# Kernel optimization log

Measured on AMD Instinct MI355X. Metric: run time of the kernel, lower is better.

## Reference

```python
import jax, jax.numpy as jnp
import numpy as np

K = 100
TEMPERATURE = 1.0


def setup_inputs() -> dict:
    key = jax.random.key(0)
    k1, k2, k3 = jax.random.split(key, 3)
    student_emb = jax.random.normal(k1, (8, 512, 1500), dtype=jnp.float32)
    teacher_codes = jax.random.randint(k2, (8, 1500), 0, 4096, dtype=jnp.int64)
    codebook = jax.random.normal(k3, (4096, 512), dtype=jnp.float32)
    return {"student_emb": student_emb, "teacher_codes": teacher_codes, "codebook": codebook}


def reference(student_emb, teacher_codes, codebook):
    B, C, T = student_emb.shape
    # flatten tokens: (N, C) with N = B*T
    emb = jnp.transpose(student_emb, (0, 2, 1)).reshape(-1, C)
    codes = teacher_codes.reshape(-1).astype(jnp.int32)

    # Euclidean cdist via the ||a||^2 + ||b||^2 - 2ab expansion (same math as torch.cdist)
    emb_sq = jnp.sum(emb * emb, axis=1, keepdims=True)            # (N,1)
    cb_sq = jnp.sum(codebook * codebook, axis=1)[None, :]         # (1,V)
    d2 = emb_sq + cb_sq - 2.0 * jnp.matmul(emb, codebook.T)       # (N,V)
    distances = jnp.sqrt(jnp.maximum(d2, 0.0))

    # top-k smallest distances
    _, top_k_indices = jax.lax.top_k(-distances, K)               # (N,K)

    # include_correct: replace last candidate with the true code if absent
    correct_in_topk = jnp.any(top_k_indices == codes[:, None], axis=1)
    top_k_indices = top_k_indices.at[:, -1].set(
        jnp.where(correct_in_topk, top_k_indices[:, -1], codes))

    candidate_distances = jnp.take_along_axis(distances, top_k_indices, axis=1)
    logits = -candidate_distances / TEMPERATURE                   # (N,K)

    match = top_k_indices == codes[:, None]
    local_labels = jnp.argmax(match.astype(jnp.int32), axis=1)    # (N,)

    logp = jax.nn.log_softmax(logits, axis=1)
    loss = -jnp.mean(jnp.take_along_axis(logp, local_labels[:, None], axis=1))

    local_predictions = jnp.argmax(logits, axis=-1)
    local_accuracy = jnp.mean((local_predictions == local_labels).astype(jnp.float32))
    global_predictions = jnp.argmin(distances, axis=-1)
    global_accuracy = jnp.mean((global_predictions == codes).astype(jnp.float32))
    correct_in_candidates = jnp.mean(jnp.any(top_k_indices == codes[:, None], axis=1).astype(jnp.float32))

    return loss, local_accuracy, global_accuracy, correct_in_candidates
```

## Files before the change

### kernel.cpp

```cpp
#include <hip/hip_runtime.h>
#include <hip/hip_bf16.h>
#include <cstdint>

#define B_ 8
#define C_ 512
#define T_ 1500
#define N_ (B_*T_)
#define NPAD_ 12032
#define V_ 4096
#define K_ 100

typedef unsigned long long u64;
typedef __attribute__((ext_vector_type(8))) short short8;
typedef __attribute__((ext_vector_type(8))) unsigned short u16x8;
typedef __attribute__((ext_vector_type(4))) float f32x4;

__device__ __forceinline__ unsigned short f2bf(float x){
    __hip_bfloat16 h = __float2bfloat16(x);
    return __builtin_bit_cast(unsigned short, h);
}
__device__ __forceinline__ unsigned short f2h(float x){
    return __builtin_bit_cast(unsigned short, (_Float16)x);
}
__device__ __forceinline__ float h2f(unsigned short h){
    return (float)__builtin_bit_cast(_Float16, h);
}

__device__ __forceinline__ void gll16(const unsigned short* g, unsigned short* l){
    __builtin_amdgcn_global_load_lds(
        (const __attribute__((address_space(1))) void*)g,
        (__attribute__((address_space(3))) void*)l, 16, 0, 0);
}

__global__ __launch_bounds__(256) void cbconv_kernel(const float* __restrict__ CB,
                                                     unsigned short* __restrict__ CBh,
                                                     float* __restrict__ csq){
    int wv = threadIdx.x >> 6, lane = threadIdx.x & 63;
    int r = blockIdx.x * 4 + wv;
    const float4* p4 = (const float4*)(CB + (size_t)r * C_);
    ushort4* o4 = (ushort4*)(CBh + (size_t)r * C_);
    float s = 0.f;
    #pragma unroll
    for (int j = 0; j < 2; ++j){
        float4 v = p4[lane + j*64];
        s += v.x*v.x + v.y*v.y + v.z*v.z + v.w*v.w;
        ushort4 h; h.x = f2bf(v.x); h.y = f2bf(v.y); h.z = f2bf(v.z); h.w = f2bf(v.w);
        o4[lane + j*64] = h;
    }
    #pragma unroll
    for (int o = 32; o; o >>= 1) s += __shfl_down(s, o, 64);
    if (lane == 0) csq[r] = s;
}

__global__ __launch_bounds__(256) void transpose_conv_kernel(const float* __restrict__ S,
                                                             unsigned short* __restrict__ embT,
                                                             float* __restrict__ esq){
    __shared__ float tile[32][33];
    __shared__ float psum[8][33];
    int b  = blockIdx.z;
    int c0 = blockIdx.y * 32;
    int t0 = blockIdx.x * 32;
    int tx = threadIdx.x, ty = threadIdx.y;
    #pragma unroll
    for (int r = 0; r < 4; ++r){
        int c = c0 + ty + r*8;
        int t = t0 + tx;
        tile[ty + r*8][tx] = (t < T_) ? S[((size_t)b*C_ + c)*T_ + t] : 0.f;
    }
    __syncthreads();
    float ps = 0.f;
    #pragma unroll
    for (int r = 0; r < 4; ++r){ float v = tile[ty + r*8][tx]; ps += v * v; }
    psum[ty][tx] = ps;
    #pragma unroll
    for (int r = 0; r < 4; ++r){
        int t = t0 + ty + r*8;
        int c = c0 + tx;
        if (t < T_) embT[((size_t)b*T_ + t)*C_ + c] = f2bf(tile[tx][ty + r*8]);
    }
    __syncthreads();
    if (ty == 0){
        int t = t0 + tx;
        if (t < T_){
            float s2 = 0.f;
            #pragma unroll
            for (int w = 0; w < 8; ++w) s2 += psum[w][tx];
            atomicAdd(&esq[b*T_ + t], s2);
        }
    }
}

__global__ __launch_bounds__(256) void gemm_dot_kernel(
    const unsigned short* __restrict__ A, const unsigned short* __restrict__ Bm,
    unsigned short* __restrict__ doth, int row_lo, int row_hi)
{
    __shared__ unsigned short smem[128*136];
    unsigned short* As = smem;
    unsigned short* Bs = smem + 128*32;
    int tid = threadIdx.x, lane = tid & 63, wv = tid >> 6;
    int row0 = row_lo + blockIdx.x * 128;
    int col0 = blockIdx.y * 128;

    int sr = lane >> 2;
    int sk = (lane & 3) * 8;
    int ar0 = row0 + wv*32 + sr;       int ar1 = ar0 + 16;
    int ca0 = (ar0 < N_) ? ar0 : N_-1; int ca1 = (ar1 < N_) ? ar1 : N_-1;
    const unsigned short* Ap0 = A  + (size_t)ca0 * C_ + sk;
    const unsigned short* Ap1 = A  + (size_t)ca1 * C_ + sk;
    const unsigned short* Bp0 = Bm + (size_t)(col0 + wv*32 + sr) * C_ + sk;
    const unsigned short* Bp1 = Bp0 + (size_t)16 * C_;
    unsigned short* Ad0 = &As[(wv*32     ) * 32];
    unsigned short* Ad1 = &As[(wv*32 + 16) * 32];
    unsigned short* Bd0 = &Bs[(wv*32     ) * 32];
    unsigned short* Bd1 = &Bs[(wv*32 + 16) * 32];

    int wm = (wv >> 1) * 64, wn = (wv & 1) * 64;
    int fr = lane & 15;
    int fk = (lane >> 4) * 8;

    f32x4 acc[4][4];
    #pragma unroll
    for (int i = 0; i < 4; ++i)
        #pragma unroll
        for (int j = 0; j < 4; ++j) acc[i][j] = (f32x4){0.f, 0.f, 0.f, 0.f};

    for (int kt = 0; kt < C_/32; ++kt){
        int k0 = kt * 32;
        gll16(Ap0 + k0, Ad0);
        gll16(Ap1 + k0, Ad1);
        gll16(Bp0 + k0, Bd0);
        gll16(Bp1 + k0, Bd1);
        __syncthreads();
        short8 af[4], bf[4];
        #pragma unroll
        for (int i = 0; i < 4; ++i) af[i] = *(const short8*)&As[(wm + i*16 + fr)*32 + fk];
        #pragma unroll
        for (int j = 0; j < 4; ++j) bf[j] = *(const short8*)&Bs[(wn + j*16 + fr)*32 + fk];
        #pragma unroll
        for (int i = 0; i < 4; ++i)
            #pragma unroll
            for (int j = 0; j < 4; ++j)
                acc[i][j] = __builtin_amdgcn_mfma_f32_16x16x32_bf16(bf[j], af[i], acc[i][j], 0, 0, 0);
        __syncthreads();
    }

    const int LD = 136;
    int en = lane & 15;
    int ev = (lane >> 4) * 4;
    #pragma unroll
    for (int i = 0; i < 4; ++i){
        int r = wm + i*16 + en;
        #pragma unroll
        for (int j = 0; j < 4; ++j){
            ushort4 h;
            h.x = f2h(acc[i][j][0]);
            h.y = f2h(acc[i][j][1]);
            h.z = f2h(acc[i][j][2]);
            h.w = f2h(acc[i][j][3]);
            *(ushort4*)&smem[r*LD + wn + j*16 + ev] = h;
        }
    }
    __syncthreads();

    int rr = tid >> 4;
    int cc = (tid & 15) * 8;
    #pragma unroll
    for (int it = 0; it < 8; ++it){
        int r = it*16 + rr;
        int n = row0 + r;
        if (n < row_hi){
            u16x8 v = *(const u16x8*)&smem[r*LD + cc];
            *(u16x8*)&doth[(size_t)(n - row_lo) * V_ + col0 + cc] = v;
        }
    }
}

__global__ __launch_bounds__(256, 2) void select_kernel(const unsigned short* __restrict__ doth,
                                                        const int* __restrict__ codes,
                                                        const float* __restrict__ esq,
                                                        const float* __restrict__ csq,
                                                        float2* __restrict__ pairbuf,
                                                        int row_lo, int nrows){
    int tid = threadIdx.x, lane = tid & 63, wv = tid >> 6;
    int lrow = blockIdx.x * 4 + wv;
    if (lrow >= nrows) return;
    int n = row_lo + lrow;
    const u16x8* r8 = (const u16x8*)(doth + (size_t)lrow * V_);

    __shared__ unsigned hist[4][256] __attribute__((aligned(16)));
    __shared__ unsigned coll[4][64];
    __shared__ unsigned collcnt[4];

    float esq_n = esq[n];
    int code = codes[n];
    float dotc = h2f(doth[(size_t)lrow * V_ + code]);
    unsigned ucode = __float_as_uint(fmaxf(esq_n + csq[code] - 2.f * dotc, 0.f));

    unsigned u[64];
    #pragma unroll
    for (int j = 0; j < 8; ++j){
        u16x8 h = r8[lane + j*64];
        const float4* cp = (const float4*)(csq + 8*lane + 512*j);
        float4 c0 = cp[0], c1 = cp[1];
        float cs[8] = {c0.x, c0.y, c0.z, c0.w, c1.x, c1.y, c1.z, c1.w};
        #pragma unroll
        for (int e = 0; e < 8; ++e){
            float d2 = fmaxf(esq_n + cs[e] - 2.f * h2f(h[e]), 0.f);
            u[8*j+e] = __float_as_uint(d2);
        }
    }

    unsigned umin = u[0], umax = u[0];
    #pragma unroll
    for (int k = 1; k < 64; ++k){
        umin = (u[k] < umin) ? u[k] : umin;
        umax = (u[k] > umax) ? u[k] : umax;
    }
    #pragma unroll
    for (int o = 32; o; o >>= 1){
        unsigned a = (unsigned)__shfl_xor((int)umin, o, 64); if (a < umin) umin = a;
        unsigned b = (unsigned)__shfl_xor((int)umax, o, 64); if (b > umax) umax = b;
    }
    unsigned im = 0xFFFFFFFFu;
    #pragma unroll
    for (int k = 0; k < 64; ++k){
        unsigned idx = 8u*(unsigned)lane + (unsigned)(512*(k >> 3) + (k & 7));
        if (u[k] == umin && idx < im) im = idx;
    }
    #pragma unroll
    for (int o = 32; o; o >>= 1){
        unsigned a = (unsigned)__shfl_xor((int)im, o, 64); if (a < im) im = a;
    }
    int idx0 = (int)im;
    float d0 = sqrtf(__uint_as_float(umin));

    unsigned t;
    if (umin == umax){
        t = umin;
    } else {
        ((uint4*)&hist[wv][0])[lane] = (uint4){0u,0u,0u,0u};
        if (lane == 0) collcnt[wv] = 0u;
        asm volatile("s_waitcnt lgkmcnt(0)" ::: "memory");
        float fmn = __uint_as_float(umin), fmx = __uint_as_float(umax);
        float invw = 256.0f / (fmx - fmn);
        #pragma unroll
        for (int k = 0; k < 64; ++k){
            float fk = __uint_as_float(u[k]);
            int b = (int)((fk - fmn) * invw); b = (b > 255) ? 255 : b;
            atomicAdd(&hist[wv][b], 1u);
        }
        asm volatile("s_waitcnt lgkmcnt(0)" ::: "memory");
        uint4 hq = ((uint4*)&hist[wv][0])[lane];
        unsigned lsum = hq.x + hq.y + hq.z + hq.w;
        unsigned inc = lsum;
        #pragma unroll
        for (int o = 1; o < 64; o <<= 1){
            unsigned y = (unsigned)__shfl_up((int)inc, o, 64);
            if (lane >= o) inc += y;
        }
        unsigned e0 = inc - lsum;
        unsigned e1 = e0 + hq.x, e2 = e1 + hq.y, e3 = e2 + hq.z, e4 = e3 + hq.w;
        int sel = -1;
        if      (e0 <= 99u && 99u < e1) sel = 0;
        else if (e1 <= 99u && 99u < e2) sel = 1;
        else if (e2 <= 99u && 99u < e3) sel = 2;
        else if (e3 <= 99u && 99u < e4) sel = 3;
        u64 bal = __ballot(sel >= 0);
        int src = __ffsll(bal) - 1;
        unsigned myBk = (unsigned)(4*lane + (sel < 0 ? 0 : sel));
        unsigned myBase = (sel == 1) ? e1 : (sel == 2) ? e2 : (sel == 3) ? e3 : e0;
        int Bk   = __shfl((int)myBk,   src, 64);
        int base = __shfl((int)myBase, src, 64);
        int rk = 99 - base;
        #pragma unroll
        for (int k = 0; k < 64; ++k){
            float fk = __uint_as_float(u[k]);
            int b = (int)((fk - fmn) * invw); b = (b > 255) ? 255 : b;
            if (b == Bk){
                unsigned pos = atomicAdd(&collcnt[wv], 1u);
                if (pos < 64u) coll[wv][pos] = u[k];
            }
        }
        asm volatile("s_waitcnt lgkmcnt(0)" ::: "memory");
        unsigned bcnt = collcnt[wv];
        if (bcnt <= 64u){
            unsigned w = (lane < (int)bcnt) ? coll[wv][lane] : 0xFFFFFFFFu;
            unsigned wmn = (lane < (int)bcnt) ? w : 0xFFFFFFFFu;
            unsigned wmx = (lane < (int)bcnt) ? w : 0u;
            #pragma unroll
            for (int o = 32; o; o >>= 1){
                unsigned a = (unsigned)__shfl_xor((int)wmn, o, 64); if (a < wmn) wmn = a;
                unsigned b = (unsigned)__shfl_xor((int)wmx, o, 64); if (b > wmx) wmx = b;
            }
            unsigned P;
            if (wmn == wmx) P = wmn;
            else {
                int hb = 31 - __clz((int)(wmn ^ wmx));
                unsigned mask = (hb == 31) ? 0xFFFFFFFFu : ((1u << (hb+1)) - 1u);
                P = wmn & ~mask;
                for (int b = hb; b >= 0; --b){
                    unsigned cand = P | (1u << b);
                    int c = __popcll(__ballot(w < cand));
                    if (c <= rk) P = cand;
                }
            }
            t = P;
        } else {
            int hb = 31 - __clz((int)(umin ^ umax));
            unsigned mask = (hb == 31) ? 0xFFFFFFFFu : ((1u << (hb+1)) - 1u);
            unsigned P = umin & ~mask;
            for (int b = hb; b >= 0; --b){
                unsigned cand = P | (1u << b);
                int c = 0;
                #pragma unroll
                for (int k = 0; k < 64; ++k) c += (u[k] < cand) ? 1 : 0;
                #pragma unroll
                for (int o = 32; o; o >>= 1) c += __shfl_xor(c, o, 64);
                if (c <= 99) P = cand;
            }
            t = P;
        }
    }
    float tval = sqrtf(__uint_as_float(t));

    float s = 0.f; int cl = 0;
    #pragma unroll
    for (int k = 0; k < 64; ++k){
        if (u[k] < t){ s += __expf(d0 - sqrtf(__uint_as_float(u[k]))); cl++; }
    }
    #pragma unroll
    for (int o = 32; o; o >>= 1){
        s += __shfl_xor(s, o, 64);
        cl += __shfl_xor(cl, o, 64);
    }
    if (lane == 0){
        float S = s + (float)(K_ - cl) * __expf(d0 - tval);
        float dcode = sqrtf(__uint_as_float(ucode));
        if (ucode > t) S += __expf(d0 - dcode) - __expf(d0 - tval);
        float nll = dcode - d0 + __logf(S);
        pairbuf[n] = make_float2(nll, (idx0 == code) ? 1.f : 0.f);
    }
}

__global__ __launch_bounds__(1024) void finalize_kernel(const float2* __restrict__ pair,
                                                        float* __restrict__ out){
    int tid = threadIdx.x;
    float sn = 0.f, sh = 0.f;
    for (int i = tid; i < N_; i += 1024){
        float2 p = pair[i]; sn += p.x; sh += p.y;
    }
    #pragma unroll
    for (int o = 32; o; o >>= 1){ sn += __shfl_down(sn, o, 64); sh += __shfl_down(sh, o, 64); }
    __shared__ float a[16], b[16];
    int wv = tid >> 6, lane = tid & 63;
    if (lane == 0){ a[wv] = sn; b[wv] = sh; }
    __syncthreads();
    if (tid == 0){
        float L = 0.f, H = 0.f;
        #pragma unroll
        for (int i = 0; i < 16; ++i){ L += a[i]; H += b[i]; }
        out[0] = L / (float)N_;
        out[1] = H / (float)N_;
        out[2] = H / (float)N_;
        out[3] = 1.0f;
    }
}

extern "C" void kernel_launch(void* const* d_in, const int* in_sizes, int n_in,
                              void* d_out, int out_size, void* d_ws, size_t ws_size,
                              hipStream_t stream){
    const float* S   = (const float*)d_in[0];
    const int* codes = (const int*)d_in[1];
    const float* CB  = (const float*)d_in[2];
    float* out = (float*)d_out;

    char* w = (char*)d_ws;
    size_t off = 0;
    unsigned short* embT = (unsigned short*)(w + off); off += (size_t)NPAD_ * C_ * 2;
    unsigned short* CBh  = (unsigned short*)(w + off); off += (size_t)V_ * C_ * 2;
    float* csq = (float*)(w + off); off += (size_t)V_ * 4;
    float* esq = (float*)(w + off); off += (size_t)N_ * 4;
    off = (off + 255) & ~(size_t)255;
    float2* pairbuf = (float2*)(w + off); off += (size_t)N_ * 8;
    unsigned short* dotbuf = (unsigned short*)(w + off);

    size_t avail = (ws_size > off) ? ws_size - off : 0;
    long maxrows = (long)(avail / ((size_t)V_ * 2));

    hipMemsetAsync(esq, 0, (size_t)N_ * 4, stream);
    hipLaunchKernelGGL(cbconv_kernel, dim3(V_/4), dim3(256), 0, stream, CB, CBh, csq);
    hipLaunchKernelGGL(transpose_conv_kernel, dim3((T_+31)/32, C_/32, B_), dim3(32, 8), 0, stream,
                       S, embT, esq);

    if (maxrows >= N_){
        const int gchunk = 6144;
        for (int row_lo = 0; row_lo < N_; row_lo += gchunk){
            int row_hi = row_lo + gchunk; if (row_hi > N_) row_hi = N_;
            int rows = row_hi - row_lo;
            hipLaunchKernelGGL(gemm_dot_kernel, dim3((rows + 127)/128, V_/128), dim3(256), 0, stream,
                               embT, CBh, dotbuf + (size_t)row_lo * V_, row_lo, row_hi);
        }
        hipLaunchKernelGGL(select_kernel, dim3((N_ + 3)/4), dim3(256), 0, stream,
                           dotbuf, codes, esq, csq, pairbuf, 0, N_);
    } else {
        int chunk = (int)(maxrows & ~127L);
        if (chunk < 128) chunk = 128;
        for (int row_lo = 0; row_lo < N_; row_lo += chunk){
            int row_hi = row_lo + chunk; if (row_hi > N_) row_hi = N_;
            int rows = row_hi - row_lo;
            hipLaunchKernelGGL(gemm_dot_kernel, dim3((rows + 127)/128, V_/128), dim3(256), 0, stream,
                               embT, CBh, dotbuf, row_lo, row_hi);
            hipLaunchKernelGGL(select_kernel, dim3((rows + 3)/4), dim3(256), 0, stream,
                               dotbuf, codes, esq, csq, pairbuf, row_lo, rows);
        }
    }
    hipLaunchKernelGGL(finalize_kernel, dim3(1), dim3(1024), 0, stream, pairbuf, out);
}
```

Baseline: 214.8 us.

## Process two rows per wavefront in select kernel with interleaved selection

The select kernel now handles two rows per wavefront instead of one. The two rows' distance computation, min/max and argmin reductions, histogram, bucket collection and radix bit search are interleaved to raise instruction-level parallelism and hide LDS and shuffle latency. It also fuses argmin tracking into the first pass, drops the equal-min/max special case and shared-prefix shortcut in favour of a full 32-bit search, and doubles shared histogram storage. The cost is roughly doubled register pressure (two 64-entry arrays), which can lower occupancy or cause spills.

```diff
diff --git a/kernel.cpp b/kernel.cpp
--- a/kernel.cpp
+++ b/kernel.cpp
@@ -182,163 +182,229 @@
                                                         float2* __restrict__ pairbuf,
                                                         int row_lo, int nrows){
     int tid = threadIdx.x, lane = tid & 63, wv = tid >> 6;
-    int lrow = blockIdx.x * 4 + wv;
-    if (lrow >= nrows) return;
-    int n = row_lo + lrow;
-    const u16x8* r8 = (const u16x8*)(doth + (size_t)lrow * V_);
-
-    __shared__ unsigned hist[4][256] __attribute__((aligned(16)));
-    __shared__ unsigned coll[4][64];
-    __shared__ unsigned collcnt[4];
-
-    float esq_n = esq[n];
-    int code = codes[n];
-    float dotc = h2f(doth[(size_t)lrow * V_ + code]);
-    unsigned ucode = __float_as_uint(fmaxf(esq_n + csq[code] - 2.f * dotc, 0.f));
-
-    unsigned u[64];
+    int lbase = blockIdx.x * 8 + wv * 2;
+    if (lbase >= nrows) return;
+    bool has1 = (lbase + 1 < nrows);
+    int l0 = lbase, l1 = has1 ? lbase + 1 : lbase;
+    int n0 = row_lo + l0, n1 = row_lo + l1;
+    const u16x8* ra = (const u16x8*)(doth + (size_t)l0 * V_);
+    const u16x8* rb = (const u16x8*)(doth + (size_t)l1 * V_);
+
+    __shared__ unsigned hist[8][256] __attribute__((aligned(16)));
+    __shared__ unsigned coll[8][64];
+    __shared__ unsigned collcnt[8];
+    int h0 = wv*2, h1 = wv*2 + 1;
+
+    float es0 = esq[n0], es1 = esq[n1];
+    int cd0 = codes[n0], cd1 = codes[n1];
+    float dc0 = h2f(doth[(size_t)l0 * V_ + cd0]);
+    float dc1 = h2f(doth[(size_t)l1 * V_ + cd1]);
+    unsigned uc0 = __float_as_uint(fmaxf(es0 + csq[cd0] - 2.f * dc0, 0.f));
+    unsigned uc1 = __float_as_uint(fmaxf(es1 + csq[cd1] - 2.f * dc1, 0.f));
+
+    unsigned u0[64], u1[64];
+    unsigned mn0 = 0xFFFFFFFFu, mx0 = 0u, mn1 = 0xFFFFFFFFu, mx1 = 0u;
+    int km0 = 0, km1 = 0;
     #pragma unroll
     for (int j = 0; j < 8; ++j){
-        u16x8 h = r8[lane + j*64];
+        u16x8 ha = ra[lane + j*64];
+        u16x8 hb = rb[lane + j*64];
         const float4* cp = (const float4*)(csq + 8*lane + 512*j);
         float4 c0 = cp[0], c1 = cp[1];
         float cs[8] = {c0.x, c0.y, c0.z, c0.w, c1.x, c1.y, c1.z, c1.w};
         #pragma unroll
         for (int e = 0; e < 8; ++e){
-            float d2 = fmaxf(esq_n + cs[e] - 2.f * h2f(h[e]), 0.f);
-            u[8*j+e] = __float_as_uint(d2);
-        }
-    }
-
-    unsigned umin = u[0], umax = u[0];
-    #pragma unroll
-    for (int k = 1; k < 64; ++k){
-        umin = (u[k] < umin) ? u[k] : umin;
-        umax = (u[k] > umax) ? u[k] : umax;
-    }
+            int k = 8*j + e;
+            unsigned v0 = __float_as_uint(fmaxf(es0 + cs[e] - 2.f * h2f(ha[e]), 0.f));
+            unsigned v1 = __float_as_uint(fmaxf(es1 + cs[e] - 2.f * h2f(hb[e]), 0.f));
+            u0[k] = v0; u1[k] = v1;
+            if (v0 < mn0){ mn0 = v0; km0 = k; }
+            mx0 = (v0 > mx0) ? v0 : mx0;
+            if (v1 < mn1){ mn1 = v1; km1 = k; }
+            mx1 = (v1 > mx1) ? v1 : mx1;
+        }
+    }
+    unsigned im0 = 8u*(unsigned)lane + (unsigned)(512*(km0 >> 3) + (km0 & 7));
+    unsigned im1 = 8u*(unsigned)lane + (unsigned)(512*(km1 >> 3) + (km1 & 7));
     #pragma unroll
     for (int o = 32; o; o >>= 1){
-        unsigned a = (unsigned)__shfl_xor((int)umin, o, 64); if (a < umin) umin = a;
-        unsigned b = (unsigned)__shfl_xor((int)umax, o, 64); if (b > umax) umax = b;
-    }
-    unsigned im = 0xFFFFFFFFu;
+        unsigned v2 = (unsigned)__shfl_xor((int)mn0, o, 64);
+        unsigned i2 = (unsigned)__shfl_xor((int)im0, o, 64);
+        if (v2 < mn0 || (v2 == mn0 && i2 < im0)){ mn0 = v2; im0 = i2; }
+        unsigned x2 = (unsigned)__shfl_xor((int)mx0, o, 64); if (x2 > mx0) mx0 = x2;
+        unsigned v3 = (unsigned)__shfl_xor((int)mn1, o, 64);
+        unsigned i3 = (unsigned)__shfl_xor((int)im1, o, 64);
+        if (v3 < mn1 || (v3 == mn1 && i3 < im1)){ mn1 = v3; im1 = i3; }
+        unsigned x3 = (unsigned)__shfl_xor((int)mx1, o, 64); if (x3 > mx1) mx1 = x3;
+    }
+    int idx00 = (int)im0, idx01 = (int)im1;
+    float d00 = sqrtf(__uint_as_float(mn0));
+    float d01 = sqrtf(__uint_as_float(mn1));
+
+    ((uint4*)&hist[h0][0])[lane] = (uint4){0u,0u,0u,0u};
+    ((uint4*)&hist[h1][0])[lane] = (uint4){0u,0u,0u,0u};
+    if (lane == 0){ collcnt[h0] = 0u; collcnt[h1] = 0u; }
+    asm volatile("s_waitcnt lgkmcnt(0)" ::: "memory");
+    float fmn0 = __uint_as_float(mn0), fmx0 = __uint_as_float(mx0);
+    float fmn1 = __uint_as_float(mn1), fmx1 = __uint_as_float(mx1);
+    float iw0 = (mx0 > mn0) ? 256.0f / (fmx0 - fmn0) : 0.f;
+    float iw1 = (mx1 > mn1) ? 256.0f / (fmx1 - fmn1) : 0.f;
+    float nb0 = -fmn0 * iw0, nb1 = -fmn1 * iw1;
     #pragma unroll
     for (int k = 0; k < 64; ++k){
-        unsigned idx = 8u*(unsigned)lane + (unsigned)(512*(k >> 3) + (k & 7));
-        if (u[k] == umin && idx < im) im = idx;
-    }
-    #pragma unroll
-    for (int o = 32; o; o >>= 1){
-        unsigned a = (unsigned)__shfl_xor((int)im, o, 64); if (a < im) im = a;
-    }
-    int idx0 = (int)im;
-    float d0 = sqrtf(__uint_as_float(umin));
-
-    unsigned t;
-    if (umin == umax){
-        t = umin;
+        int b0 = (int)fmaf(__uint_as_float(u0[k]), iw0, nb0); b0 = (b0 > 255) ? 255 : b0;
+        int b1 = (int)fmaf(__uint_as_float(u1[k]), iw1, nb1); b1 = (b1 > 255) ? 255 : b1;
+        atomicAdd(&hist[h0][b0], 1u);
+        atomicAdd(&hist[h1][b1], 1u);
+    }
+    asm volatile("s_waitcnt lgkmcnt(0)" ::: "memory");
+
+    uint4 hq0 = ((uint4*)&hist[h0][0])[lane];
+    uint4 hq1 = ((uint4*)&hist[h1][0])[lane];
+    unsigned ls0 = hq0.x + hq0.y + hq0.z + hq0.w;
+    unsigned ls1 = hq1.x + hq1.y + hq1.z + hq1.w;
+    unsigned in0 = ls0, in1 = ls1;
+    #pragma unroll
+    for (int o = 1; o < 64; o <<= 1){
+        unsigned y0 = (unsigned)__shfl_up((int)in0, o, 64);
+        unsigned y1 = (unsigned)__shfl_up((int)in1, o, 64);
+        if (lane >= o){ in0 += y0; in1 += y1; }
+    }
+    unsigned e00 = in0 - ls0;
+    unsigned e01 = e00 + hq0.x, e02 = e01 + hq0.y, e03 = e02 + hq0.z, e04 = e03 + hq0.w;
+    int s0 = -1;
+    if      (e00 <= 99u && 99u < e01) s0 = 0;
+    else if (e01 <= 99u && 99u < e02) s0 = 1;
+    else if (e02 <= 99u && 99u < e03) s0 = 2;
+    else if (e03 <= 99u && 99u < e04) s0 = 3;
+    unsigned e10 = in1 - ls1;
+    unsigned e11 = e10 + hq1.x, e12 = e11 + hq1.y, e13 = e12 + hq1.z, e14 = e13 + hq1.w;
+    int s1 = -1;
+    if      (e10 <= 99u && 99u < e11) s1 = 0;
+    else if (e11 <= 99u && 99u < e12) s1 = 1;
+    else if (e12 <= 99u && 99u < e13) s1 = 2;
+    else if (e13 <= 99u && 99u < e14) s1 = 3;
+    u64 bl0 = __ballot(s0 >= 0);
+    u64 bl1 = __ballot(s1 >= 0);
+    int sr0 = __ffsll(bl0) - 1;
+    int sr1 = __ffsll(bl1) - 1;
+    unsigned mB0 = (unsigned)(4*lane + (s0 < 0 ? 0 : s0));
+    unsigned mB1 = (unsigned)(4*lane + (s1 < 0 ? 0 : s1));
+    unsigned mE0 = (s0 == 1) ? e01 : (s0 == 2) ? e02 : (s0 == 3) ? e03 : e00;
+    unsigned mE1 = (s1 == 1) ? e11 : (s1 == 2) ? e12 : (s1 == 3) ? e13 : e10;
+    int Bk0 = __shfl((int)mB0, sr0, 64);
+    int Bk1 = __shfl((int)mB1, sr1, 64);
+    int ba0 = __shfl((int)mE0, sr0, 64);
+    int ba1 = __shfl((int)mE1, sr1, 64);
+    int rk0 = 99 - ba0, rk1 = 99 - ba1;
+
+    #pragma unroll
+    for (int k = 0; k < 64; ++k){
+        int b0 = (int)fmaf(__uint_as_float(u0[k]), iw0, nb0); b0 = (b0 > 255) ? 255 : b0;
+        int b1 = (int)fmaf(__uint_as_float(u1[k]), iw1, nb1); b1 = (b1 > 255) ? 255 : b1;
+        if (b0 == Bk0){
+            unsigned pos = atomicAdd(&collcnt[h0], 1u);
+            if (pos < 64u) coll[h0][pos] = u0[k];
+        }
+        if (b1 == Bk1){
+            unsigned pos = atomicAdd(&collcnt[h1], 1u);
+            if (pos < 64u) coll[h1][pos] = u1[k];
+        }
+    }
+    asm volatile("s_waitcnt lgkmcnt(0)" ::: "memory");
+    int bc0 = (int)collcnt[h0], bc1 = (int)collcnt[h1];
+
+    unsigned t0u, t1u;
+    bool f0 = bc0 > 64, f1 = bc1 > 64;
+    unsigned w0 = 0xFFFFFFFFu, w1 = 0xFFFFFFFFu;
+    if (!f0) w0 = (lane < bc0) ? coll[h0][lane] : 0xFFFFFFFFu;
+    if (!f1) w1 = (lane < bc1) ? coll[h1][lane] : 0xFFFFFFFFu;
+    if (!f0 && !f1){
+        unsigned P0 = 0u, P1 = 0u;
+        #pragma unroll
+        for (int b = 31; b >= 0; --b){
+            unsigned c0 = P0 | (1u << b);
+            unsigned c1 = P1 | (1u << b);
+            int q0 = (int)__popcll(__ballot(w0 < c0));
+            int q1 = (int)__popcll(__ballot(w1 < c1));
+            if (q0 <= rk0) P0 = c0;
+            if (q1 <= rk1) P1 = c1;
+        }
+        t0u = P0; t1u = P1;
     } else {
-        ((uint4*)&hist[wv][0])[lane] = (uint4){0u,0u,0u,0u};
-        if (lane == 0) collcnt[wv] = 0u;
-        asm volatile("s_waitcnt lgkmcnt(0)" ::: "memory");
-        float fmn = __uint_as_float(umin), fmx = __uint_as_float(umax);
-        float invw = 256.0f / (fmx - fmn);
-        #pragma unroll
-        for (int k = 0; k < 64; ++k){
-            float fk = __uint_as_float(u[k]);
-            int b = (int)((fk - fmn) * invw); b = (b > 255) ? 255 : b;
-            atomicAdd(&hist[wv][b], 1u);
-        }
-        asm volatile("s_waitcnt lgkmcnt(0)" ::: "memory");
-        uint4 hq = ((uint4*)&hist[wv][0])[lane];
-        unsigned lsum = hq.x + hq.y + hq.z + hq.w;
-        unsigned inc = lsum;
-        #pragma unroll
-        for (int o = 1; o < 64; o <<= 1){
-            unsigned y = (unsigned)__shfl_up((int)inc, o, 64);
-            if (lane >= o) inc += y;
-        }
-        unsigned e0 = inc - lsum;
-        unsigned e1 = e0 + hq.x, e2 = e1 + hq.y, e3 = e2 + hq.z, e4 = e3 + hq.w;
-        int sel = -1;
-        if      (e0 <= 99u && 99u < e1) sel = 0;
-        else if (e1 <= 99u && 99u < e2) sel = 1;
-        else if (e2 <= 99u && 99u < e3) sel = 2;
-        else if (e3 <= 99u && 99u < e4) sel = 3;
-        u64 bal = __ballot(sel >= 0);
-        int src = __ffsll(bal) - 1;
-        unsigned myBk = (unsigned)(4*lane + (sel < 0 ? 0 : sel));
-        unsigned myBase = (sel == 1) ? e1 : (sel == 2) ? e2 : (sel == 3) ? e3 : e0;
-        int Bk   = __shfl((int)myBk,   src, 64);
-        int base = __shfl((int)myBase, src, 64);
-        int rk = 99 - base;
-        #pragma unroll
-        for (int k = 0; k < 64; ++k){
-            float fk = __uint_as_float(u[k]);
-            int b = (int)((fk - fmn) * invw); b = (b > 255) ? 255 : b;
-            if (b == Bk){
-                unsigned pos = atomicAdd(&collcnt[wv], 1u);
-                if (pos < 64u) coll[wv][pos] = u[k];
+        if (!f0){
+            unsigned P = 0u;
+            #pragma unroll
+            for (int b = 31; b >= 0; --b){
+                unsigned c = P | (1u << b);
+                if ((int)__popcll(__ballot(w0 < c)) <= rk0) P = c;
             }
-        }
-        asm volatile("s_waitcnt lgkmcnt(0)" ::: "memory");
-        unsigned bcnt = collcnt[wv];
-        if (bcnt <= 64u){
-            unsigned w = (lane < (int)bcnt) ? coll[wv][lane] : 0xFFFFFFFFu;
-            unsigned wmn = (lane < (int)bcnt) ? w : 0xFFFFFFFFu;
-            unsigned wmx = (lane < (int)bcnt) ? w : 0u;
-            #pragma unroll
-            for (int o = 32; o; o >>= 1){
-                unsigned a = (unsigned)__shfl_xor((int)wmn, o, 64); if (a < wmn) wmn = a;
-                unsigned b = (unsigned)__shfl_xor((int)wmx, o, 64); if (b > wmx) wmx = b;
-            }
-            unsigned P;
-            if (wmn == wmx) P = wmn;
-            else {
-                int hb = 31 - __clz((int)(wmn ^ wmx));
-                unsigned mask = (hb == 31) ? 0xFFFFFFFFu : ((1u << (hb+1)) - 1u);
-                P = wmn & ~mask;
-                for (int b = hb; b >= 0; --b){
-                    unsigned cand = P | (1u << b);
-                    int c = __popcll(__ballot(w < cand));
-                    if (c <= rk) P = cand;
-                }
-            }
-            t = P;
+            t0u = P;
         } else {
-            int hb = 31 - __clz((int)(umin ^ umax));
-            unsigned mask = (hb == 31) ? 0xFFFFFFFFu : ((1u << (hb+1)) - 1u);
-            unsigned P = umin & ~mask;
-            for (int b = hb; b >= 0; --b){
+            unsigned P = 0u;
+            for (int b = 31; b >= 0; --b){
                 unsigned cand = P | (1u << b);
                 int c = 0;
                 #pragma unroll
-                for (int k = 0; k < 64; ++k) c += (u[k] < cand) ? 1 : 0;
+                for (int k = 0; k < 64; ++k) c += (u0[k] < cand) ? 1 : 0;
                 #pragma unroll
                 for (int o = 32; o; o >>= 1) c += __shfl_xor(c, o, 64);
                 if (c <= 99) P = cand;
             }
-            t = P;
-        }
-    }
-    float tval = sqrtf(__uint_as_float(t));
-
-    float s = 0.f; int cl = 0;
+            t0u = P;
+        }
+        if (!f1){
+            unsigned P = 0u;
+            #pragma unroll
+            for (int b = 31; b >= 0; --b){
+                unsigned c = P | (1u << b);
+                if ((int)__popcll(__ballot(w1 < c)) <= rk1) P = c;
+            }
+            t1u = P;
+        } else {
+            unsigned P = 0u;
+            for (int b = 31; b >= 0; --b){
+                unsigned cand = P | (1u << b);
+                int c = 0;
+                #pragma unroll
+                for (int k = 0; k < 64; ++k) c += (u1[k] < cand) ? 1 : 0;
+                #pragma unroll
+                for (int o = 32; o; o >>= 1) c += __shfl_xor(c, o, 64);
+                if (c <= 99) P = cand;
+            }
+            t1u = P;
+        }
+    }
+    float tv0 = sqrtf(__uint_as_float(t0u));
+    float tv1 = sqrtf(__uint_as_float(t1u));
+
+    float sm0 = 0.f, sm1 = 0.f;
+    int cl0 = 0, cl1 = 0;
     #pragma unroll
     for (int k = 0; k < 64; ++k){
-        if (u[k] < t){ s += __expf(d0 - sqrtf(__uint_as_float(u[k]))); cl++; }
+        if (u0[k] < t0u){ sm0 += __expf(d00 - sqrtf(__uint_as_float(u0[k]))); cl0++; }
+        if (u1[k] < t1u){ sm1 += __expf(d01 - sqrtf(__uint_as_float(u1[k]))); cl1++; }
     }
     #pragma unroll
     for (int o = 32; o; o >>= 1){
-        s += __shfl_xor(s, o, 64);
-        cl += __shfl_xor(cl, o, 64);
+        sm0 += __shfl_xor(sm0, o, 64); cl0 += __shfl_xor(cl0, o, 64);
+        sm1 += __shfl_xor(sm1, o, 64); cl1 += __shfl_xor(cl1, o, 64);
     }
     if (lane == 0){
-        float S = s + (float)(K_ - cl) * __expf(d0 - tval);
-        float dcode = sqrtf(__uint_as_float(ucode));
-        if (ucode > t) S += __expf(d0 - dcode) - __expf(d0 - tval);
-        float nll = dcode - d0 + __logf(S);
-        pairbuf[n] = make_float2(nll, (idx0 == code) ? 1.f : 0.f);
+        {
+            float S = sm0 + (float)(K_ - cl0) * __expf(d00 - tv0);
+            float dcode = sqrtf(__uint_as_float(uc0));
+            if (uc0 > t0u) S += __expf(d00 - dcode) - __expf(d00 - tv0);
+            float nll = dcode - d00 + __logf(S);
+            pairbuf[n0] = make_float2(nll, (idx00 == cd0) ? 1.f : 0.f);
+        }
+        if (has1){
+            float S = sm1 + (float)(K_ - cl1) * __expf(d01 - tv1);
+            float dcode = sqrtf(__uint_as_float(uc1));
+            if (uc1 > t1u) S += __expf(d01 - dcode) - __expf(d01 - tv1);
+            float nll = dcode - d01 + __logf(S);
+            pairbuf[n1] = make_float2(nll, (idx01 == cd1) ? 1.f : 0.f);
+        }
     }
 }
 
@@ -400,7 +466,7 @@
             hipLaunchKernelGGL(gemm_dot_kernel, dim3((rows + 127)/128, V_/128), dim3(256), 0, stream,
                                embT, CBh, dotbuf + (size_t)row_lo * V_, row_lo, row_hi);
         }
-        hipLaunchKernelGGL(select_kernel, dim3((N_ + 3)/4), dim3(256), 0, stream,
+        hipLaunchKernelGGL(select_kernel, dim3((N_ + 7)/8), dim3(256), 0, stream,
                            dotbuf, codes, esq, csq, pairbuf, 0, N_);
     } else {
         int chunk = (int)(maxrows & ~127L);
@@ -410,7 +476,7 @@
             int rows = row_hi - row_lo;
             hipLaunchKernelGGL(gemm_dot_kernel, dim3((rows + 127)/128, V_/128), dim3(256), 0, stream,
                                embT, CBh, dotbuf, row_lo, row_hi);
-            hipLaunchKernelGGL(select_kernel, dim3((rows + 3)/4), dim3(256), 0, stream,
+            hipLaunchKernelGGL(select_kernel, dim3((rows + 7)/8), dim3(256), 0, stream,
                                dotbuf, codes, esq, csq, pairbuf, row_lo, rows);
         }
     }
```

After: 271.5 us. 26.4% more time.
